# Kernel tuning notes

Hardware: AMD Instinct MI355X
Metric: run time of the kernel (lower is better)

## Reference

```python
import jax, jax.numpy as jnp
import numpy as np

NUM_REGIONS = 20
EMBED_DIM = 768
PATCH = (4, 16, 16)          # (pd, ph, pw)
IMG = (64, 512, 512)         # (D, H, W)
B = 2
N_PATCHES = 16384


def setup_inputs() -> dict:
    key = jax.random.key(0)
    k1, k2, k3 = jax.random.split(key, 3)
    segmentation_mask = jax.random.randint(
        k1, (B, 1) + IMG, 0, NUM_REGIONS + 1, dtype=jnp.int32)
    patch_coords = jax.random.uniform(k2, (B, N_PATCHES, 3), dtype=jnp.float32)
    region_prototypes = 0.02 * jax.random.normal(
        k3, (NUM_REGIONS, EMBED_DIM), dtype=jnp.float32)
    return {"segmentation_mask": segmentation_mask,
            "patch_coords": patch_coords,
            "region_prototypes": region_prototypes}


def _compute_assignments(segmentation_mask, patch_coords):
    Bsz, _, D, H, W = segmentation_mask.shape
    pd, ph, pw = PATCH
    dims = jnp.array([D, H, W], dtype=jnp.float32)
    half = jnp.array([pd // 2, ph // 2, pw // 2], dtype=jnp.float32)

    cpix = patch_coords * dims                                   # (B,N,3)
    # torch: z_start = max(0, int(c - half)); z_end = min(D, int(c + half))
    start = jnp.maximum(0.0, jnp.floor(cpix - half)).astype(jnp.int32)   # (B,N,3)
    end = jnp.minimum(dims, jnp.floor(cpix + half)).astype(jnp.int32)    # (B,N,3)

    # per-axis index grids of fixed size, validity mask honors clipped box
    zi = start[..., 0:1] + jnp.arange(pd, dtype=jnp.int32)        # (B,N,pd)
    yi = start[..., 1:2] + jnp.arange(ph, dtype=jnp.int32)        # (B,N,ph)
    xi = start[..., 2:3] + jnp.arange(pw, dtype=jnp.int32)        # (B,N,pw)
    vz = zi < end[..., 0:1]
    vy = yi < end[..., 1:2]
    vx = xi < end[..., 2:3]

    ziC = jnp.clip(zi, 0, D - 1)
    yiC = jnp.clip(yi, 0, H - 1)
    xiC = jnp.clip(xi, 0, W - 1)

    # flattened gather: (B, N, pd, ph, pw) voxel values
    lin = (ziC[:, :, :, None, None] * (H * W)
           + yiC[:, :, None, :, None] * W
           + xiC[:, :, None, None, :])
    flat = segmentation_mask.reshape(Bsz, D * H * W)
    vals = jnp.take_along_axis(flat, lin.reshape(Bsz, -1), axis=1)
    vals = vals.reshape(Bsz, lin.shape[1], pd, ph, pw)
    valid = (vz[:, :, :, None, None]
             & vy[:, :, None, :, None]
             & vx[:, :, None, None, :])

    # numel of each (possibly clipped) crop
    extents = jnp.maximum(end - start, 0)                         # (B,N,3)
    numel = jnp.prod(extents, axis=-1).astype(jnp.float32)        # (B,N)

    # per-region counts; small fixed loop over 20 regions keeps memory low
    counts = jnp.stack(
        [jnp.sum((vals == r) & valid, axis=(2, 3, 4)).astype(jnp.float32)
         for r in range(1, NUM_REGIONS + 1)], axis=-1)            # (B,N,R)

    prop = counts / jnp.maximum(numel, 1.0)[..., None]            # zero crops -> 0
    a = prop + 1e-6
    a = a / jnp.sum(a, axis=-1, keepdims=True)
    return a


def reference(segmentation_mask, patch_coords, region_prototypes):
    Bsz = segmentation_mask.shape[0]
    region_features = jnp.broadcast_to(
        region_prototypes[None], (Bsz,) + region_prototypes.shape)
    patch_to_region = _compute_assignments(segmentation_mask, patch_coords)
    return region_features, patch_to_region
```

## Files before the change

kernel.cpp:

```cpp
#include <hip/hip_runtime.h>

#define NREG   20
#define EDIM   768
#define DVOL   64
#define HVOL   512
#define WVOL   512
#define HW_    (HVOL * WVOL)
#define DHW_   (DVOL * HVOL * WVOL)
#define NPATCH 16384
#define BTOT   2
#define PROTO_N (NREG * EDIM)
#define RF_N    (BTOT * PROTO_N)
#define TOTAL_PATCHES (BTOT * NPATCH)

struct __attribute__((packed, aligned(4))) int4p { int x, y, z, w; };

__global__ __launch_bounds__(256) void assign_kernel(
    const int*   __restrict__ seg,
    const float* __restrict__ coords,
    const float* __restrict__ proto,
    float*       __restrict__ out)
{
    __shared__ unsigned smem[4][8][5];

    if (blockIdx.x < RF_N / 256) {
        const int i = blockIdx.x * 256 + threadIdx.x;
        out[i] = proto[i >= PROTO_N ? i - PROTO_N : i];
    }

    const int lane  = threadIdx.x & 63;
    const int wave  = threadIdx.x >> 6;
    const int patch = blockIdx.x * 4 + wave;
    const int b     = patch >> 14;

    const float c0 = coords[patch * 3 + 0] * 64.0f;
    const float c1 = coords[patch * 3 + 1] * 512.0f;
    const float c2 = coords[patch * 3 + 2] * 512.0f;

    const int sz = (int)fmaxf(0.0f,   floorf(c0 - 2.0f));
    const int ez = (int)fminf(64.0f,  floorf(c0 + 2.0f));
    const int sy = (int)fmaxf(0.0f,   floorf(c1 - 8.0f));
    const int ey = (int)fminf(512.0f, floorf(c1 + 8.0f));
    const int sx = (int)fmaxf(0.0f,   floorf(c2 - 8.0f));
    const int ex = (int)fminf(512.0f, floorf(c2 + 8.0f));

    const int xl4  = lane & 3;
    const int yy   = lane >> 2;
    const int p_lo = sx + 4 * xl4;
    const int st   = min(p_lo, WVOL - 4);
    const int yi   = sy + yy;
    const unsigned vy = (yi < ey) ? 0xFFFFFFFFu : 0u;
    const int yiC  = min(yi, HVOL - 1);
    const int rowbase = b * DHW_ + yiC * WVOL + st;

    unsigned vm[4];
#pragma unroll
    for (int j = 0; j < 4; ++j) {
        const int pos = st + j;
        vm[j] = (pos >= p_lo && pos < ex) ? vy : 0u;
    }

    int4p q0, q1, q2, q3;
    {
        const int z0 = min(sz + 0, DVOL - 1) * HW_;
        const int z1 = min(sz + 1, DVOL - 1) * HW_;
        const int z2 = min(sz + 2, DVOL - 1) * HW_;
        const int z3 = min(sz + 3, DVOL - 1) * HW_;
        q0 = *(const int4p*)(seg + rowbase + z0);
        q1 = *(const int4p*)(seg + rowbase + z1);
        q2 = *(const int4p*)(seg + rowbase + z2);
        q3 = *(const int4p*)(seg + rowbase + z3);
    }

    unsigned cc[5] = {0u, 0u, 0u, 0u, 0u};

#pragma unroll
    for (int z = 0; z < 4; ++z) {
        const unsigned zm = (sz + z < ez) ? 0xFFFFFFFFu : 0u;
        const int4p qz = (z == 0) ? q0 : (z == 1) ? q1 : (z == 2) ? q2 : q3;
        const int vals[4] = {qz.x, qz.y, qz.z, qz.w};
#pragma unroll
        for (int j = 0; j < 4; ++j) {
            const int v = vals[j] & (int)(vm[j] & zm);
            const int t = v - 1;
            const unsigned inc = 1u << ((t & 3) << 3);
            const int qk = t >> 2;
#pragma unroll
            for (int k = 0; k < 5; ++k)
                cc[k] += (qk == k) ? inc : 0u;
        }
    }

#pragma unroll
    for (int off = 1; off < 8; off <<= 1) {
#pragma unroll
        for (int k = 0; k < 5; ++k)
            cc[k] += (unsigned)__shfl_xor((int)cc[k], off);
    }

    if ((lane & 7) == 0) {
#pragma unroll
        for (int k = 0; k < 5; ++k)
            smem[wave][lane >> 3][k] = cc[k];
    }
    __syncthreads();

    const float nz = (float)max(ez - sz, 0);
    const float ny = (float)max(ey - sy, 0);
    const float nx = (float)max(ex - sx, 0);
    const float numel = nz * ny * nx;
    const float denom = fmaxf(numel, 1.0f);

    unsigned cnt = 0u;
    if (lane < NREG) {
        const int k  = lane >> 2;
        const int sh = (lane & 3) * 8;
#pragma unroll
        for (int g = 0; g < 8; ++g)
            cnt += (smem[wave][g][k] >> sh) & 0xFFu;
    }

    unsigned tot = cnt;
#pragma unroll
    for (int off = 1; off < 32; off <<= 1)
        tot += (unsigned)__shfl_xor((int)tot, off);

    if (lane < NREG) {
        const float s = (float)tot / denom + (float)NREG * 1e-6f;
        const float a = (float)cnt / denom + 1e-6f;
        out[RF_N + patch * NREG + lane] = a / s;
    }
}

extern "C" void kernel_launch(void* const* d_in, const int* in_sizes, int n_in,
                              void* d_out, int out_size, void* d_ws, size_t ws_size,
                              hipStream_t stream)
{
    const int*   seg    = (const int*)d_in[0];
    const float* coords = (const float*)d_in[1];
    const float* proto  = (const float*)d_in[2];
    float*       out    = (float*)d_out;

    hipLaunchKernelGGL(assign_kernel, dim3(TOTAL_PATCHES / 4), dim3(256), 0, stream,
                       seg, coords, proto, out);
}
```

Before: 59.54 us.

## Bucket-sort patches by spatial bin and swizzle blocks for cache locality

```diff
diff --git a/kernel.cpp b/kernel.cpp
--- a/kernel.cpp
+++ b/kernel.cpp
@@ -12,30 +12,89 @@
 #define PROTO_N (NREG * EDIM)
 #define RF_N    (BTOT * PROTO_N)
 #define TOTAL_PATCHES (BTOT * NPATCH)
+#define NBUCKET 1024
+
+#define WS_COUNTS  0
+#define WS_OFFSETS 1024
+#define WS_KEYS    2048
+#define WS_PID     (2048 + TOTAL_PATCHES)
+#define WS_C0      (WS_PID + TOTAL_PATCHES)
+#define WS_C1      (WS_C0  + TOTAL_PATCHES)
+#define WS_C2      (WS_C1  + TOTAL_PATCHES)
 
 struct __attribute__((packed, aligned(4))) int4p { int x, y, z, w; };
+
+__global__ __launch_bounds__(1024) void zero_counts_kernel(unsigned* __restrict__ ws)
+{
+    ws[WS_COUNTS + threadIdx.x] = 0u;
+}
+
+__global__ __launch_bounds__(256) void count_kernel(
+    const float* __restrict__ coords, unsigned* __restrict__ ws)
+{
+    const int p = blockIdx.x * 256 + threadIdx.x;
+    const int b = p >> 14;
+    const float zf = coords[p * 3 + 0] * 64.0f;
+    const float yf = coords[p * 3 + 1] * 512.0f;
+    const int zbin = min(31, ((int)zf) >> 1);
+    const int ybin = min(15, ((int)yf) >> 5);
+    const unsigned key = (unsigned)(b * 512 + zbin * 16 + ybin);
+    ws[WS_KEYS + p] = key;
+    atomicAdd(&ws[WS_COUNTS + key], 1u);
+}
+
+__global__ __launch_bounds__(1024) void scan_kernel(unsigned* __restrict__ ws)
+{
+    __shared__ unsigned tmp[NBUCKET];
+    const int t = threadIdx.x;
+    const unsigned v = ws[WS_COUNTS + t];
+    tmp[t] = v;
+    __syncthreads();
+#pragma unroll
+    for (int off = 1; off < NBUCKET; off <<= 1) {
+        const unsigned y = (t >= off) ? tmp[t - off] : 0u;
+        __syncthreads();
+        tmp[t] += y;
+        __syncthreads();
+    }
+    ws[WS_OFFSETS + t] = tmp[t] - v;
+}
+
+__global__ __launch_bounds__(256) void scatter_kernel(
+    const float* __restrict__ coords, unsigned* __restrict__ ws)
+{
+    const int p = blockIdx.x * 256 + threadIdx.x;
+    const unsigned key  = ws[WS_KEYS + p];
+    const unsigned rank = atomicAdd(&ws[WS_OFFSETS + key], 1u);
+    ws[WS_PID + rank] = (unsigned)p;
+    ((float*)ws)[WS_C0 + rank] = coords[p * 3 + 0];
+    ((float*)ws)[WS_C1 + rank] = coords[p * 3 + 1];
+    ((float*)ws)[WS_C2 + rank] = coords[p * 3 + 2];
+}
 
 __global__ __launch_bounds__(256) void assign_kernel(
     const int*   __restrict__ seg,
-    const float* __restrict__ coords,
+    const unsigned* __restrict__ ws,
     const float* __restrict__ proto,
     float*       __restrict__ out)
 {
-    __shared__ unsigned smem[4][8][5];
-
     if (blockIdx.x < RF_N / 256) {
         const int i = blockIdx.x * 256 + threadIdx.x;
         out[i] = proto[i >= PROTO_N ? i - PROTO_N : i];
     }
 
-    const int lane  = threadIdx.x & 63;
-    const int wave  = threadIdx.x >> 6;
-    const int patch = blockIdx.x * 4 + wave;
-    const int b     = patch >> 14;
-
-    const float c0 = coords[patch * 3 + 0] * 64.0f;
-    const float c1 = coords[patch * 3 + 1] * 512.0f;
-    const float c2 = coords[patch * 3 + 2] * 512.0f;
+    const int bid  = (int)blockIdx.x;
+    const int sbid = (bid & 7) * 1024 + (bid >> 3);
+
+    const int lane = threadIdx.x & 63;
+    const int wave = threadIdx.x >> 6;
+    const int slot = sbid * 4 + wave;
+
+    const int   patch = (int)ws[WS_PID + slot];
+    const float c0 = ((const float*)ws)[WS_C0 + slot] * 64.0f;
+    const float c1 = ((const float*)ws)[WS_C1 + slot] * 512.0f;
+    const float c2 = ((const float*)ws)[WS_C2 + slot] * 512.0f;
+    const int b = patch >> 14;
 
     const int sz = (int)fmaxf(0.0f,   floorf(c0 - 2.0f));
     const int ez = (int)fminf(64.0f,  floorf(c0 + 2.0f));
@@ -73,7 +132,6 @@
     }
 
     unsigned cc[5] = {0u, 0u, 0u, 0u, 0u};
-
 #pragma unroll
     for (int z = 0; z < 4; ++z) {
         const unsigned zm = (sz + z < ez) ? 0xFFFFFFFFu : 0u;
@@ -98,34 +156,39 @@
             cc[k] += (unsigned)__shfl_xor((int)cc[k], off);
     }
 
-    if ((lane & 7) == 0) {
-#pragma unroll
-        for (int k = 0; k < 5; ++k)
-            smem[wave][lane >> 3][k] = cc[k];
-    }
-    __syncthreads();
-
-    const float nz = (float)max(ez - sz, 0);
-    const float ny = (float)max(ey - sy, 0);
-    const float nx = (float)max(ex - sx, 0);
-    const float numel = nz * ny * nx;
-    const float denom = fmaxf(numel, 1.0f);
-
-    unsigned cnt = 0u;
+    unsigned lo[5], hi[5];
+#pragma unroll
+    for (int k = 0; k < 5; ++k) {
+        lo[k] = cc[k] & 0x00FF00FFu;
+        hi[k] = (cc[k] >> 8) & 0x00FF00FFu;
+    }
+#pragma unroll
+    for (int off = 8; off < 64; off <<= 1) {
+#pragma unroll
+        for (int k = 0; k < 5; ++k) {
+            lo[k] += (unsigned)__shfl_xor((int)lo[k], off);
+            hi[k] += (unsigned)__shfl_xor((int)hi[k], off);
+        }
+    }
+
+    unsigned S = 0u;
+#pragma unroll
+    for (int k = 0; k < 5; ++k) S += lo[k] + hi[k];
+    const unsigned tot = (S & 0xFFFFu) + (S >> 16);
+
+    const int r = lane & 3;
+    const unsigned sLo = (lane < 4) ? lo[0] : (lane < 8) ? lo[1]
+                       : (lane < 12) ? lo[2] : (lane < 16) ? lo[3] : lo[4];
+    const unsigned sHi = (lane < 4) ? hi[0] : (lane < 8) ? hi[1]
+                       : (lane < 12) ? hi[2] : (lane < 16) ? hi[3] : hi[4];
+    const unsigned fld = (r & 1) ? sHi : sLo;
+    const unsigned cnt = (r & 2) ? (fld >> 16) : (fld & 0xFFFFu);
+
     if (lane < NREG) {
-        const int k  = lane >> 2;
-        const int sh = (lane & 3) * 8;
-#pragma unroll
-        for (int g = 0; g < 8; ++g)
-            cnt += (smem[wave][g][k] >> sh) & 0xFFu;
-    }
-
-    unsigned tot = cnt;
-#pragma unroll
-    for (int off = 1; off < 32; off <<= 1)
-        tot += (unsigned)__shfl_xor((int)tot, off);
-
-    if (lane < NREG) {
+        const float nz = (float)max(ez - sz, 0);
+        const float ny = (float)max(ey - sy, 0);
+        const float nx = (float)max(ex - sx, 0);
+        const float denom = fmaxf(nz * ny * nx, 1.0f);
         const float s = (float)tot / denom + (float)NREG * 1e-6f;
         const float a = (float)cnt / denom + 1e-6f;
         out[RF_N + patch * NREG + lane] = a / s;
@@ -140,7 +203,14 @@
     const float* coords = (const float*)d_in[1];
     const float* proto  = (const float*)d_in[2];
     float*       out    = (float*)d_out;
-
+    unsigned*    ws     = (unsigned*)d_ws;
+
+    hipLaunchKernelGGL(zero_counts_kernel, dim3(1), dim3(NBUCKET), 0, stream, ws);
+    hipLaunchKernelGGL(count_kernel, dim3(TOTAL_PATCHES / 256), dim3(256), 0, stream,
+                       coords, ws);
+    hipLaunchKernelGGL(scan_kernel, dim3(1), dim3(NBUCKET), 0, stream, ws);
+    hipLaunchKernelGGL(scatter_kernel, dim3(TOTAL_PATCHES / 256), dim3(256), 0, stream,
+                       coords, ws);
     hipLaunchKernelGGL(assign_kernel, dim3(TOTAL_PATCHES / 4), dim3(256), 0, stream,
-                       seg, coords, proto, out);
-}
+                       seg, ws, proto, out);
+}
```

Result: faster. 55.48 us (-6.8%).

## Bucket-sort patches by spatial region and remap blocks for cache locality

Applied to the files above, without the earlier changes.

```diff
diff --git a/kernel.cpp b/kernel.cpp
--- a/kernel.cpp
+++ b/kernel.cpp
@@ -12,30 +12,94 @@
 #define PROTO_N (NREG * EDIM)
 #define RF_N    (BTOT * PROTO_N)
 #define TOTAL_PATCHES (BTOT * NPATCH)
+#define CHUNK   4096
+
+#define WS_PID 0
+#define WS_C0  (WS_PID + TOTAL_PATCHES)
+#define WS_C1  (WS_C0  + TOTAL_PATCHES)
+#define WS_C2  (WS_C1  + TOTAL_PATCHES)
 
 struct __attribute__((packed, aligned(4))) int4p { int x, y, z, w; };
 
+template<int CTRL, int RM>
+__device__ __forceinline__ unsigned dppadd(unsigned x)
+{
+    return x + (unsigned)__builtin_amdgcn_update_dpp(0, (int)x, CTRL, RM, 0xF, true);
+}
+
+__global__ __launch_bounds__(1024) void sort_kernel(
+    const float* __restrict__ coords, unsigned* __restrict__ ws)
+{
+    __shared__ unsigned counts[512], offs[512];
+    const int t  = threadIdx.x;
+    const int p0 = (int)blockIdx.x * CHUNK + t * 4;
+
+    if (t < 512) counts[t] = 0u;
+    __syncthreads();
+
+    float c[12];
+    {
+        const float4* cp = (const float4*)(coords + p0 * 3);
+        const float4 a = cp[0], b = cp[1], d = cp[2];
+        c[0]=a.x; c[1]=a.y; c[2]=a.z;  c[3]=a.w; c[4]=b.x; c[5]=b.y;
+        c[6]=b.z; c[7]=b.w; c[8]=d.x;  c[9]=d.y; c[10]=d.z; c[11]=d.w;
+    }
+    unsigned key[4];
+#pragma unroll
+    for (int i = 0; i < 4; ++i) {
+        const int zb = ((int)(c[3*i + 0] * 64.0f))  >> 1;
+        const int yb = ((int)(c[3*i + 1] * 512.0f)) >> 5;
+        key[i] = (unsigned)(zb * 16 + yb);
+        atomicAdd(&counts[key[i]], 1u);
+    }
+    __syncthreads();
+
+    if (t < 512) offs[t] = counts[t];
+    __syncthreads();
+#pragma unroll
+    for (int off = 1; off < 512; off <<= 1) {
+        const unsigned v = (t >= off && t < 512) ? offs[t - off] : 0u;
+        __syncthreads();
+        if (t < 512) offs[t] += v;
+        __syncthreads();
+    }
+    if (t < 512) offs[t] -= counts[t];
+    __syncthreads();
+
+#pragma unroll
+    for (int i = 0; i < 4; ++i) {
+        const unsigned rank = (unsigned)blockIdx.x * CHUNK
+                            + atomicAdd(&offs[key[i]], 1u);
+        ws[WS_PID + rank] = (unsigned)(p0 + i);
+        ((float*)ws)[WS_C0 + rank] = c[3*i + 0];
+        ((float*)ws)[WS_C1 + rank] = c[3*i + 1];
+        ((float*)ws)[WS_C2 + rank] = c[3*i + 2];
+    }
+}
+
 __global__ __launch_bounds__(256) void assign_kernel(
-    const int*   __restrict__ seg,
-    const float* __restrict__ coords,
-    const float* __restrict__ proto,
-    float*       __restrict__ out)
-{
-    __shared__ unsigned smem[4][8][5];
-
+    const int*      __restrict__ seg,
+    const unsigned* __restrict__ ws,
+    const float*    __restrict__ proto,
+    float*          __restrict__ out)
+{
     if (blockIdx.x < RF_N / 256) {
         const int i = blockIdx.x * 256 + threadIdx.x;
         out[i] = proto[i >= PROTO_N ? i - PROTO_N : i];
     }
 
-    const int lane  = threadIdx.x & 63;
-    const int wave  = threadIdx.x >> 6;
-    const int patch = blockIdx.x * 4 + wave;
-    const int b     = patch >> 14;
-
-    const float c0 = coords[patch * 3 + 0] * 64.0f;
-    const float c1 = coords[patch * 3 + 1] * 512.0f;
-    const float c2 = coords[patch * 3 + 2] * 512.0f;
+    const int bid  = (int)blockIdx.x;
+    const int sbid = (bid & 7) * 1024 + (bid >> 3);
+
+    const int lane = threadIdx.x & 63;
+    const int wave = threadIdx.x >> 6;
+    const int slot = sbid * 4 + wave;
+
+    const int   patch = (int)ws[WS_PID + slot];
+    const float c0 = ((const float*)ws)[WS_C0 + slot] * 64.0f;
+    const float c1 = ((const float*)ws)[WS_C1 + slot] * 512.0f;
+    const float c2 = ((const float*)ws)[WS_C2 + slot] * 512.0f;
+    const int b = patch >> 14;
 
     const int sz = (int)fmaxf(0.0f,   floorf(c0 - 2.0f));
     const int ez = (int)fminf(64.0f,  floorf(c0 + 2.0f));
@@ -73,7 +137,6 @@
     }
 
     unsigned cc[5] = {0u, 0u, 0u, 0u, 0u};
-
 #pragma unroll
     for (int z = 0; z < 4; ++z) {
         const unsigned zm = (sz + z < ez) ? 0xFFFFFFFFu : 0u;
@@ -92,40 +155,53 @@
     }
 
 #pragma unroll
-    for (int off = 1; off < 8; off <<= 1) {
-#pragma unroll
-        for (int k = 0; k < 5; ++k)
-            cc[k] += (unsigned)__shfl_xor((int)cc[k], off);
-    }
-
-    if ((lane & 7) == 0) {
-#pragma unroll
-        for (int k = 0; k < 5; ++k)
-            smem[wave][lane >> 3][k] = cc[k];
-    }
-    __syncthreads();
-
-    const float nz = (float)max(ez - sz, 0);
-    const float ny = (float)max(ey - sy, 0);
-    const float nx = (float)max(ex - sx, 0);
-    const float numel = nz * ny * nx;
-    const float denom = fmaxf(numel, 1.0f);
+    for (int k = 0; k < 5; ++k) {
+        cc[k] = dppadd<0x111, 0xF>(cc[k]);
+        cc[k] = dppadd<0x112, 0xF>(cc[k]);
+        cc[k] = dppadd<0x114, 0xF>(cc[k]);
+    }
+    unsigned lo[5], hi[5];
+#pragma unroll
+    for (int k = 0; k < 5; ++k) {
+        lo[k] = cc[k] & 0x00FF00FFu;
+        hi[k] = (cc[k] >> 8) & 0x00FF00FFu;
+    }
+#pragma unroll
+    for (int k = 0; k < 5; ++k) {
+        lo[k] = dppadd<0x118, 0xF>(lo[k]);
+        hi[k] = dppadd<0x118, 0xF>(hi[k]);
+        lo[k] = dppadd<0x142, 0xA>(lo[k]);
+        hi[k] = dppadd<0x142, 0xA>(hi[k]);
+        lo[k] = dppadd<0x143, 0xC>(lo[k]);
+        hi[k] = dppadd<0x143, 0xC>(hi[k]);
+    }
+
+    unsigned cl[5], ch[5];
+#pragma unroll
+    for (int k = 0; k < 5; ++k) {
+        cl[k] = (unsigned)__builtin_amdgcn_readlane((int)lo[k], 63);
+        ch[k] = (unsigned)__builtin_amdgcn_readlane((int)hi[k], 63);
+    }
+
+    unsigned S = 0u;
+#pragma unroll
+    for (int k = 0; k < 5; ++k) S += cl[k] + ch[k];
+    const unsigned tot = (S & 0xFFFFu) + (S >> 16);
 
     unsigned cnt = 0u;
+#pragma unroll
+    for (int k = 0; k < 5; ++k) {
+        cnt = (lane == 4*k + 0) ? (cl[k] & 0xFFFFu) : cnt;
+        cnt = (lane == 4*k + 1) ? (ch[k] & 0xFFFFu) : cnt;
+        cnt = (lane == 4*k + 2) ? (cl[k] >> 16)     : cnt;
+        cnt = (lane == 4*k + 3) ? (ch[k] >> 16)     : cnt;
+    }
+
     if (lane < NREG) {
-        const int k  = lane >> 2;
-        const int sh = (lane & 3) * 8;
-#pragma unroll
-        for (int g = 0; g < 8; ++g)
-            cnt += (smem[wave][g][k] >> sh) & 0xFFu;
-    }
-
-    unsigned tot = cnt;
-#pragma unroll
-    for (int off = 1; off < 32; off <<= 1)
-        tot += (unsigned)__shfl_xor((int)tot, off);
-
-    if (lane < NREG) {
+        const float nz = (float)max(ez - sz, 0);
+        const float ny = (float)max(ey - sy, 0);
+        const float nx = (float)max(ex - sx, 0);
+        const float denom = fmaxf(nz * ny * nx, 1.0f);
         const float s = (float)tot / denom + (float)NREG * 1e-6f;
         const float a = (float)cnt / denom + 1e-6f;
         out[RF_N + patch * NREG + lane] = a / s;
@@ -140,7 +216,10 @@
     const float* coords = (const float*)d_in[1];
     const float* proto  = (const float*)d_in[2];
     float*       out    = (float*)d_out;
-
-    hipLaunchKernelGGL(assign_kernel, dim3(TOTAL_PATCHES / 4), dim3(256), 0, stream,
-                       seg, coords, proto, out);
-}
+    unsigned*    ws     = (unsigned*)d_ws;
+
+    hipLaunchKernelGGL(sort_kernel, dim3(TOTAL_PATCHES / CHUNK), dim3(1024),
+                       0, stream, coords, ws);
+    hipLaunchKernelGGL(assign_kernel, dim3(TOTAL_PATCHES / 4), dim3(256),
+                       0, stream, seg, ws, proto, out);
+}
```

New measurement: 57.36 us. -3.7%, faster.
